# Optimization experiments

Hardware: AMD Instinct MI355X
Metric: run time of the kernel (lower is better)

## Reference

```python
import jax, jax.numpy as jnp
import numpy as np

F_IN = 10000
M = 3
CARD = 5
LOG_2PI = float(np.log(2.0 * np.pi))


def _normal_logprob(x, means, stds):
    # x: [N, F, 1]; means/stds: [1, F, M] -> [N, F, M]
    z = (x - means) / stds
    return -0.5 * (z * z) - jnp.log(stds) - 0.5 * LOG_2PI


def _sum_layer(x, w):
    # x: [N, F, Cin]; w: [F, Cin, Cout] -> [N, F, Cout]
    logw = jax.nn.log_softmax(w, axis=1)
    return jax.scipy.special.logsumexp(x[:, :, :, None] + logw[None], axis=2)


def _product_layer(x, card):
    # log-domain product = segmented sum over blocks of `card` features
    n, f, c = x.shape
    return x.reshape(n, f // card, card, c).sum(axis=2)


def setup_inputs() -> dict:
    key = jax.random.key(0)
    ks = jax.random.split(key, 9)
    x = jax.random.normal(ks[0], (4096, F_IN), dtype=jnp.float32)
    means = jax.random.normal(ks[1], (1, F_IN, M), dtype=jnp.float32)
    stds = jax.random.uniform(ks[2], (1, F_IN, M), dtype=jnp.float32, minval=0.5, maxval=1.5)
    w1 = jax.random.normal(ks[3], (F_IN, M, 1), dtype=jnp.float32)
    w2 = jax.random.normal(ks[4], (F_IN // 5, 1, 1), dtype=jnp.float32)
    w3 = jax.random.normal(ks[5], (F_IN // 25, 1, 1), dtype=jnp.float32)
    w4 = jax.random.normal(ks[6], (F_IN // 125, 1, 1), dtype=jnp.float32)
    w5 = jax.random.normal(ks[7], (F_IN // 625, 1, 1), dtype=jnp.float32)
    rand_idxs = jax.random.permutation(ks[8], F_IN).astype(jnp.int32)
    return {"x": x, "means": means, "stds": stds, "w1": w1, "w2": w2,
            "w3": w3, "w4": w4, "w5": w5, "rand_idxs": rand_idxs}


def reference(x, means, stds, w1, w2, w3, w4, w5, rand_idxs):
    # scope permutation gather
    xp = x[:, rand_idxs]                          # [N, F]
    y = _normal_logprob(xp[:, :, None], means, stds)  # [N, F, M]
    y = _sum_layer(y, w1)                          # [N, F, 1]
    y = _product_layer(y, CARD)                    # [N, F/5, 1]
    y = _sum_layer(y, w2)
    y = _product_layer(y, CARD)                    # [N, F/25, 1]
    y = _sum_layer(y, w3)
    y = _product_layer(y, CARD)                    # [N, F/125, 1]
    y = _sum_layer(y, w4)
    y = _product_layer(y, CARD)                    # [N, F/625, 1]
    y = _sum_layer(y, w5)
    y = _product_layer(y, F_IN // 5 ** 4)          # [N, 1, 1]
    return y
```

## Files before the change

kernel.cpp:

```cpp
#include <hip/hip_runtime.h>
#include <math.h>

#define F_IN 10000
#define NROWS 4096
#define CGROUPS 8
#define CH_PER_CG 5
#define RPW 2
#define ROWBLOCKS 512

typedef float v4f __attribute__((ext_vector_type(4)));

__global__ void spn_prep_kernel(const float* __restrict__ means,
                                const float* __restrict__ stds,
                                const float* __restrict__ w1,
                                const int* __restrict__ rand_idxs,
                                float* __restrict__ ws,
                                float* __restrict__ out) {
    int f = blockIdx.x * blockDim.x + threadIdx.x;
    if (f < NROWS) out[f] = 0.0f;
    if (f >= F_IN) return;

    int j = rand_idxs[f];

    float wa = w1[f * 3 + 0];
    float wb = w1[f * 3 + 1];
    float wc = w1[f * 3 + 2];
    float wm = fmaxf(fmaxf(wa, wb), wc);
    float lse = wm + __logf(__expf(wa - wm) + __expf(wb - wm) + __expf(wc - wm));

    const float INV_SQRT2 = 0.70710678118654752440f;
    const float HALF_LOG_2PI = 0.91893853320467274178f;

#pragma unroll
    for (int m = 0; m < 3; m++) {
        float w  = w1[f * 3 + m] - lse;
        float sd = stds[f * 3 + m];
        float mu = means[f * 3 + m];
        float a  = INV_SQRT2 / sd;
        float b  = -mu * a;
        float c  = w - __logf(sd) - HALF_LOG_2PI;
        ws[(0 + m) * F_IN + j] = a;
        ws[(3 + m) * F_IN + j] = b;
        ws[(6 + m) * F_IN + j] = c;
    }
}

__device__ __forceinline__ void col_term(float xv,
                                         float a0, float b0, float c0,
                                         float a1, float b1, float c1,
                                         float a2, float b2, float c2,
                                         float& mx_out, float& s_out) {
    float u0 = fmaf(xv, a0, b0);
    float u1 = fmaf(xv, a1, b1);
    float u2 = fmaf(xv, a2, b2);
    float v0 = fmaf(-u0, u0, c0);
    float v1 = fmaf(-u1, u1, c1);
    float v2 = fmaf(-u2, u2, c2);
    float mx = fmaxf(fmaxf(v0, v1), v2);
    float me = __builtin_amdgcn_fmed3f(v0, v1, v2);
    float mn = fminf(fminf(v0, v1), v2);
    float s  = 1.0f + __expf(me - mx) + __expf(mn - mx);
    mx_out = mx;
    s_out  = s;
}

__global__ __launch_bounds__(256) void spn_main_kernel(const float* __restrict__ x,
                                                       const float* __restrict__ ws,
                                                       float* __restrict__ out) {
    const int wave = threadIdx.x >> 6;
    const int lane = threadIdx.x & 63;
    const int rb   = blockIdx.x >> 3;
    const int cg   = blockIdx.x & 7;
    const int row0 = rb * (RPW * 4) + wave * RPW;
    const float* xr0 = x + (size_t)row0 * F_IN;

    float accm[RPW], prod[RPW];
#pragma unroll
    for (int r = 0; r < RPW; r++) { accm[r] = 0.0f; prod[r] = 1.0f; }

    v4f xv[RPW];
    {
        int jc = cg * 256 + lane * 4;
#pragma unroll
        for (int r = 0; r < RPW; r++)
            xv[r] = *(const v4f*)(xr0 + (size_t)r * F_IN + jc);
    }

#pragma unroll
    for (int it = 0; it < CH_PER_CG; ++it) {
        const int c = cg + it * 8;
        const int jcur = c * 256 + lane * 4;
        const bool vcur = (jcur < F_IN);
        const int q = vcur ? (jcur >> 2) : 0;

        const v4f A0 = ((const v4f*)(ws + 0 * F_IN))[q];
        const v4f A1 = ((const v4f*)(ws + 1 * F_IN))[q];
        const v4f A2 = ((const v4f*)(ws + 2 * F_IN))[q];
        const v4f B0 = ((const v4f*)(ws + 3 * F_IN))[q];
        const v4f B1 = ((const v4f*)(ws + 4 * F_IN))[q];
        const v4f B2 = ((const v4f*)(ws + 5 * F_IN))[q];
        const v4f C0 = ((const v4f*)(ws + 6 * F_IN))[q];
        const v4f C1 = ((const v4f*)(ws + 7 * F_IN))[q];
        const v4f C2 = ((const v4f*)(ws + 8 * F_IN))[q];

        v4f xn[RPW];
        if (it < CH_PER_CG - 1) {
            int jn = (c + 8) * 256 + lane * 4;
            int jnc = (jn < F_IN) ? jn : 0;
#pragma unroll
            for (int r = 0; r < RPW; r++)
                xn[r] = *(const v4f*)(xr0 + (size_t)r * F_IN + jnc);
        }

#pragma unroll
        for (int r = 0; r < RPW; r++) {
            float m0, s0, m1, s1, m2, s2, m3, s3;
            col_term(xv[r].x, A0.x, B0.x, C0.x, A1.x, B1.x, C1.x, A2.x, B2.x, C2.x, m0, s0);
            col_term(xv[r].y, A0.y, B0.y, C0.y, A1.y, B1.y, C1.y, A2.y, B2.y, C2.y, m1, s1);
            col_term(xv[r].z, A0.z, B0.z, C0.z, A1.z, B1.z, C1.z, A2.z, B2.z, C2.z, m2, s2);
            col_term(xv[r].w, A0.w, B0.w, C0.w, A1.w, B1.w, C1.w, A2.w, B2.w, C2.w, m3, s3);

            float smx = (m0 + m1) + (m2 + m3);
            float sp  = (s0 * s1) * (s2 * s3);
            accm[r] += vcur ? smx : 0.0f;
            prod[r] *= vcur ? sp : 1.0f;
        }

        if (it < CH_PER_CG - 1) {
#pragma unroll
            for (int r = 0; r < RPW; r++) xv[r] = xn[r];
        }
    }

#pragma unroll
    for (int r = 0; r < RPW; r++) {
        float part = accm[r] + __logf(prod[r]);
#pragma unroll
        for (int off = 32; off > 0; off >>= 1)
            part += __shfl_xor(part, off, 64);
        if (lane == 0)
            atomicAdd(&out[row0 + r], part);
    }
}

extern "C" void kernel_launch(void* const* d_in, const int* in_sizes, int n_in,
                              void* d_out, int out_size, void* d_ws, size_t ws_size,
                              hipStream_t stream) {
    const float* x         = (const float*)d_in[0];
    const float* means     = (const float*)d_in[1];
    const float* stds      = (const float*)d_in[2];
    const float* w1        = (const float*)d_in[3];
    const int*   rand_idxs = (const int*)d_in[8];

    float* out = (float*)d_out;
    float* ws  = (float*)d_ws;

    spn_prep_kernel<<<(F_IN + 255) / 256, 256, 0, stream>>>(means, stds, w1, rand_idxs, ws, out);

    spn_main_kernel<<<ROWBLOCKS * CGROUPS, 256, 0, stream>>>(x, ws, out);
}
```

Before: 264.8 us.

## Swap work decomposition: each block owns one column chunk, iterates over rows

Each block now takes one 256-column chunk and 64 rows, with every wave covering 16 rows. The nine per-column coefficient vectors are loaded once per thread and reused across all 16 rows, where before each thread reloaded them for each of 5 column chunks. The cost is many more atomics: one per row per chunk (40 per output) instead of one per row per column group (8). There is also a lane reduction and a log for every row rather than a single accumulated product.

After: 251.8 us. 4.9% less time.

```diff
diff --git a/kernel.cpp b/kernel.cpp
--- a/kernel.cpp
+++ b/kernel.cpp
@@ -3,10 +3,9 @@
 
 #define F_IN 10000
 #define NROWS 4096
-#define CGROUPS 8
-#define CH_PER_CG 5
-#define RPW 2
-#define ROWBLOCKS 512
+#define NCHUNK 40
+#define RSLICES 64
+#define ROWS_PER_WAVE 16
 
 typedef float v4f __attribute__((ext_vector_type(4)));
 
@@ -69,77 +68,62 @@
                                                        float* __restrict__ out) {
     const int wave = threadIdx.x >> 6;
     const int lane = threadIdx.x & 63;
-    const int rb   = blockIdx.x >> 3;
-    const int cg   = blockIdx.x & 7;
-    const int row0 = rb * (RPW * 4) + wave * RPW;
-    const float* xr0 = x + (size_t)row0 * F_IN;
+    const int c    = blockIdx.x >> 6;
+    const int rs   = blockIdx.x & 63;
 
-    float accm[RPW], prod[RPW];
+    const int col  = c * 256 + lane * 4;
+    const bool vld = (col < F_IN);
+    const int q    = vld ? (col >> 2) : 0;
+
+    const v4f A0 = ((const v4f*)(ws + 0 * F_IN))[q];
+    const v4f A1 = ((const v4f*)(ws + 1 * F_IN))[q];
+    const v4f A2 = ((const v4f*)(ws + 2 * F_IN))[q];
+    const v4f B0 = ((const v4f*)(ws + 3 * F_IN))[q];
+    const v4f B1 = ((const v4f*)(ws + 4 * F_IN))[q];
+    const v4f B2 = ((const v4f*)(ws + 5 * F_IN))[q];
+    const v4f C0 = ((const v4f*)(ws + 6 * F_IN))[q];
+    const v4f C1 = ((const v4f*)(ws + 7 * F_IN))[q];
+    const v4f C2 = ((const v4f*)(ws + 8 * F_IN))[q];
+
+    const int row0 = rs * 64 + wave * ROWS_PER_WAVE;
+    const float* xp = x + (size_t)row0 * F_IN + (vld ? col : 0);
+
+    v4f xv[4], xn[4];
 #pragma unroll
-    for (int r = 0; r < RPW; r++) { accm[r] = 0.0f; prod[r] = 1.0f; }
-
-    v4f xv[RPW];
-    {
-        int jc = cg * 256 + lane * 4;
-#pragma unroll
-        for (int r = 0; r < RPW; r++)
-            xv[r] = *(const v4f*)(xr0 + (size_t)r * F_IN + jc);
-    }
+    for (int r = 0; r < 4; r++)
+        xv[r] = *(const v4f*)(xp + (size_t)r * F_IN);
 
 #pragma unroll
-    for (int it = 0; it < CH_PER_CG; ++it) {
-        const int c = cg + it * 8;
-        const int jcur = c * 256 + lane * 4;
-        const bool vcur = (jcur < F_IN);
-        const int q = vcur ? (jcur >> 2) : 0;
-
-        const v4f A0 = ((const v4f*)(ws + 0 * F_IN))[q];
-        const v4f A1 = ((const v4f*)(ws + 1 * F_IN))[q];
-        const v4f A2 = ((const v4f*)(ws + 2 * F_IN))[q];
-        const v4f B0 = ((const v4f*)(ws + 3 * F_IN))[q];
-        const v4f B1 = ((const v4f*)(ws + 4 * F_IN))[q];
-        const v4f B2 = ((const v4f*)(ws + 5 * F_IN))[q];
-        const v4f C0 = ((const v4f*)(ws + 6 * F_IN))[q];
-        const v4f C1 = ((const v4f*)(ws + 7 * F_IN))[q];
-        const v4f C2 = ((const v4f*)(ws + 8 * F_IN))[q];
-
-        v4f xn[RPW];
-        if (it < CH_PER_CG - 1) {
-            int jn = (c + 8) * 256 + lane * 4;
-            int jnc = (jn < F_IN) ? jn : 0;
+    for (int j = 0; j < 4; ++j) {
+        if (j < 3) {
 #pragma unroll
-            for (int r = 0; r < RPW; r++)
-                xn[r] = *(const v4f*)(xr0 + (size_t)r * F_IN + jnc);
+            for (int r = 0; r < 4; r++)
+                xn[r] = *(const v4f*)(xp + (size_t)((j + 1) * 4 + r) * F_IN);
         }
 
 #pragma unroll
-        for (int r = 0; r < RPW; r++) {
+        for (int r = 0; r < 4; r++) {
             float m0, s0, m1, s1, m2, s2, m3, s3;
             col_term(xv[r].x, A0.x, B0.x, C0.x, A1.x, B1.x, C1.x, A2.x, B2.x, C2.x, m0, s0);
             col_term(xv[r].y, A0.y, B0.y, C0.y, A1.y, B1.y, C1.y, A2.y, B2.y, C2.y, m1, s1);
             col_term(xv[r].z, A0.z, B0.z, C0.z, A1.z, B1.z, C1.z, A2.z, B2.z, C2.z, m2, s2);
             col_term(xv[r].w, A0.w, B0.w, C0.w, A1.w, B1.w, C1.w, A2.w, B2.w, C2.w, m3, s3);
 
-            float smx = (m0 + m1) + (m2 + m3);
-            float sp  = (s0 * s1) * (s2 * s3);
-            accm[r] += vcur ? smx : 0.0f;
-            prod[r] *= vcur ? sp : 1.0f;
+            float accm = (m0 + m1) + (m2 + m3);
+            float sp   = (s0 * s1) * (s2 * s3);
+            float part = vld ? (accm + __logf(sp)) : 0.0f;
+
+#pragma unroll
+            for (int off = 32; off > 0; off >>= 1)
+                part += __shfl_xor(part, off, 64);
+            if (lane == 0)
+                atomicAdd(&out[row0 + j * 4 + r], part);
         }
 
-        if (it < CH_PER_CG - 1) {
+        if (j < 3) {
 #pragma unroll
-            for (int r = 0; r < RPW; r++) xv[r] = xn[r];
+            for (int r = 0; r < 4; r++) xv[r] = xn[r];
         }
-    }
-
-#pragma unroll
-    for (int r = 0; r < RPW; r++) {
-        float part = accm[r] + __logf(prod[r]);
-#pragma unroll
-        for (int off = 32; off > 0; off >>= 1)
-            part += __shfl_xor(part, off, 64);
-        if (lane == 0)
-            atomicAdd(&out[row0 + r], part);
     }
 }
 
@@ -157,5 +141,5 @@
 
     spn_prep_kernel<<<(F_IN + 255) / 256, 256, 0, stream>>>(means, stds, w1, rand_idxs, ws, out);
 
-    spn_main_kernel<<<ROWBLOCKS * CGROUPS, 256, 0, stream>>>(x, ws, out);
+    spn_main_kernel<<<NCHUNK * RSLICES, 256, 0, stream>>>(x, ws, out);
 }
```
